# Optimization experiments

Measured on AMD Instinct MI355X. Metric: run time of the kernel, lower is better.

The kernel has to match this reference:

```python
import jax, jax.numpy as jnp
import numpy as np

D = 256
H = 8
FFN = 2048
EPS = 1e-5


def _layer_norm(x, g, b):
    m = jnp.mean(x, axis=-1, keepdims=True)
    v = jnp.mean((x - m) ** 2, axis=-1, keepdims=True)
    return (x - m) * jax.lax.rsqrt(v + EPS) * g + b


def _mha(q_in, k_in, v_in, wq, bq, wk, bk, wv, bv, wo, bo, mask):
    B, Sq, _ = q_in.shape
    Sk = k_in.shape[1]
    dh = D // H
    q = (q_in @ wq + bq).reshape(B, Sq, H, dh)
    k = (k_in @ wk + bk).reshape(B, Sk, H, dh)
    v = (v_in @ wv + bv).reshape(B, Sk, H, dh)
    scores = jnp.einsum('bqhd,bkhd->bhqk', q, k) / jnp.sqrt(jnp.float32(dh)).astype(q.dtype)
    if mask is not None:
        scores = scores + mask
    probs = jax.nn.softmax(scores, axis=-1)
    ctx = jnp.einsum('bhqk,bkhd->bqhd', probs, v).reshape(B, Sq, D)
    return ctx @ wo + bo


def setup_inputs() -> dict:
    key = jax.random.key(0)
    ks = jax.random.split(key, 32)
    s = 0.02
    def lin(i, din, dout):
        return jax.random.normal(ks[i], (din, dout), jnp.float32) * s
    inp = {
        'vision_encoder_hidden_states': jax.random.normal(ks[0], (4, 2048, D), jnp.float32),
        'text_encoder_hidden_states': jax.random.normal(ks[1], (4, 1024, D), jnp.float32),
        'vision_encoder_attention_mask': jnp.zeros((4, 1, 1, 2048), jnp.float32),
        'text_encoder_attention_mask': jnp.zeros((4, 1, 1, 1024), jnp.float32),
        'sa_wq': lin(2, D, D), 'sa_bq': jnp.zeros((D,), jnp.float32),
        'sa_wk': lin(3, D, D), 'sa_bk': jnp.zeros((D,), jnp.float32),
        'sa_wv': lin(4, D, D), 'sa_bv': jnp.zeros((D,), jnp.float32),
        'sa_wo': lin(5, D, D), 'sa_bo': jnp.zeros((D,), jnp.float32),
        'ca_wq': lin(6, D, D), 'ca_bq': jnp.zeros((D,), jnp.float32),
        'ca_wk': lin(7, D, D), 'ca_bk': jnp.zeros((D,), jnp.float32),
        'ca_wv': lin(8, D, D), 'ca_bv': jnp.zeros((D,), jnp.float32),
        'ca_wo': lin(9, D, D), 'ca_bo': jnp.zeros((D,), jnp.float32),
        'ln1_g': jnp.ones((D,), jnp.float32), 'ln1_b': jnp.zeros((D,), jnp.float32),
        'ln2_g': jnp.ones((D,), jnp.float32), 'ln2_b': jnp.zeros((D,), jnp.float32),
        'ln3_g': jnp.ones((D,), jnp.float32), 'ln3_b': jnp.zeros((D,), jnp.float32),
        'ln4_g': jnp.ones((D,), jnp.float32), 'ln4_b': jnp.zeros((D,), jnp.float32),
        'fc1_w': lin(10, D, FFN), 'fc1_b': jnp.zeros((FFN,), jnp.float32),
        'fc2_w': lin(11, FFN, D), 'fc2_b': jnp.zeros((D,), jnp.float32),
    }
    return inp


def reference(vision_encoder_hidden_states, text_encoder_hidden_states,
              vision_encoder_attention_mask, text_encoder_attention_mask,
              sa_wq, sa_bq, sa_wk, sa_bk, sa_wv, sa_bv, sa_wo, sa_bo,
              ca_wq, ca_bq, ca_wk, ca_bk, ca_wv, ca_bv, ca_wo, ca_bo,
              ln1_g, ln1_b, ln2_g, ln2_b, ln3_g, ln3_b, ln4_g, ln4_b,
              fc1_w, fc1_b, fc2_w, fc2_b):
    # self-attention over vision queries (dropout = identity in eval)
    residual = vision_encoder_hidden_states
    h = _mha(vision_encoder_hidden_states, vision_encoder_hidden_states,
             vision_encoder_hidden_states,
             sa_wq, sa_bq, sa_wk, sa_bk, sa_wv, sa_bv, sa_wo, sa_bo,
             vision_encoder_attention_mask)
    h = _layer_norm(residual + h, ln1_g, ln1_b)
    # text cross-attention
    res2 = h
    h = _mha(h, text_encoder_hidden_states, text_encoder_hidden_states,
             ca_wq, ca_bq, ca_wk, ca_bk, ca_wv, ca_bv, ca_wo, ca_bo,
             text_encoder_attention_mask)
    h = _layer_norm(res2 + h, ln2_g, ln2_b)
    # third block: residual + dropout(h) -> in eval this is h + h = 2h, then LN
    h = _layer_norm(h + h, ln3_g, ln3_b)
    # FFN
    res = h
    h = jax.nn.relu(h @ fc1_w + fc1_b)
    h = h @ fc2_w + fc2_b
    h = _layer_norm(res + h, ln4_g, ln4_b)
    return h
```

## Files before the change

### kernel.cpp

```cpp
#include <hip/hip_runtime.h>
#include <stdint.h>
#include <stddef.h>

#define HEADS 8
#define DH 32
#define DMODEL 256
#define LN_EPS 1e-5f
#define QSCALE 0.17677669529663687f

typedef unsigned short u16;
typedef __bf16 bf16x8 __attribute__((ext_vector_type(8)));
typedef unsigned short u16x8 __attribute__((ext_vector_type(8)));
typedef float f32x4 __attribute__((ext_vector_type(4)));

static __device__ __forceinline__ u16 bfc(float f) {
    return __builtin_bit_cast(u16, (__bf16)f);
}
static __device__ __forceinline__ bf16x8 ldbf8(const u16* p) {
    return __builtin_bit_cast(bf16x8, *reinterpret_cast<const u16x8*>(p));
}
static __device__ __forceinline__ bf16x8 cvt8(float4 a, float4 b) {
    bf16x8 r;
    r[0] = (__bf16)a.x; r[1] = (__bf16)a.y; r[2] = (__bf16)a.z; r[3] = (__bf16)a.w;
    r[4] = (__bf16)b.x; r[5] = (__bf16)b.y; r[6] = (__bf16)b.z; r[7] = (__bf16)b.w;
    return r;
}

struct TDesc { const float* src; u16* dst; int K; int N; };
struct TArgs { TDesc d[10]; };

__global__ __launch_bounds__(256) void transpose_cvt(TArgs args) {
    TDesc d = args.d[blockIdx.y];
    const int ntx = d.N >> 5;
    const int tiles = (d.K >> 5) * ntx;
    if ((int)blockIdx.x >= tiles) return;
    const int tk = (blockIdx.x / ntx) << 5;
    const int tn = (blockIdx.x % ntx) << 5;
    __shared__ float t[32][33];
    const int lx = threadIdx.x & 31;
    const int ly = threadIdx.x >> 5;
#pragma unroll
    for (int i = 0; i < 4; ++i)
        t[ly + 8 * i][lx] = d.src[(size_t)(tk + ly + 8 * i) * d.N + tn + lx];
    __syncthreads();
#pragma unroll
    for (int i = 0; i < 4; ++i)
        d.dst[(size_t)(tn + ly + 8 * i) * d.K + tk + lx] = bfc(t[lx][ly + 8 * i]);
}

struct Slice { u16* out; const float* bias; int mode; float sc; };

__global__ __launch_bounds__(256) void gemm_xproj(
    const float* __restrict__ Af, const u16* __restrict__ Wt,
    Slice s0, Slice s1, Slice s2, int M, int ntm)
{
    const int lane = threadIdx.x & 63;
    const int wave = threadIdx.x >> 6;
    const int l15 = lane & 15, lhi = lane >> 4;
    const int tm = ((int)blockIdx.x % ntm) * 128;
    const int tn = ((int)blockIdx.x / ntm) * 64;
    const int wm = tm + wave * 32;
    const int sel = tn >> 8;
    const int tl = tn & 255;
    Slice sl = (sel == 0) ? s0 : (sel == 1 ? s1 : s2);

    const f32x4 z4 = {0.f, 0.f, 0.f, 0.f};
    f32x4 acc[2][4];
#pragma unroll
    for (int i = 0; i < 2; ++i)
#pragma unroll
        for (int j = 0; j < 4; ++j) acc[i][j] = z4;

    const float* ar0 = Af + (size_t)(wm + l15) * 256 + lhi * 8;
    const float* ar1 = ar0 + (size_t)16 * 256;
    const u16* b0p = Wt + (size_t)(tn + l15) * 256 + lhi * 8;

    float4 a00 = *(const float4*)(ar0), a01 = *(const float4*)(ar0 + 4);
    float4 a10 = *(const float4*)(ar1), a11 = *(const float4*)(ar1 + 4);
    bf16x8 b[4];
#pragma unroll
    for (int j = 0; j < 4; ++j) b[j] = ldbf8(b0p + (size_t)j * 16 * 256);

#pragma unroll
    for (int k = 32; k < 256; k += 32) {
        float4 n00 = *(const float4*)(ar0 + k), n01 = *(const float4*)(ar0 + k + 4);
        float4 n10 = *(const float4*)(ar1 + k), n11 = *(const float4*)(ar1 + k + 4);
        bf16x8 bn[4];
#pragma unroll
        for (int j = 0; j < 4; ++j) bn[j] = ldbf8(b0p + (size_t)j * 16 * 256 + k);
        bf16x8 a0 = cvt8(a00, a01), a1 = cvt8(a10, a11);
#pragma unroll
        for (int j = 0; j < 4; ++j) {
            acc[0][j] = __builtin_amdgcn_mfma_f32_16x16x32_bf16(a0, b[j], acc[0][j], 0, 0, 0);
            acc[1][j] = __builtin_amdgcn_mfma_f32_16x16x32_bf16(a1, b[j], acc[1][j], 0, 0, 0);
        }
        a00 = n00; a01 = n01; a10 = n10; a11 = n11;
#pragma unroll
        for (int j = 0; j < 4; ++j) b[j] = bn[j];
    }
    {
        bf16x8 a0 = cvt8(a00, a01), a1 = cvt8(a10, a11);
#pragma unroll
        for (int j = 0; j < 4; ++j) {
            acc[0][j] = __builtin_amdgcn_mfma_f32_16x16x32_bf16(a0, b[j], acc[0][j], 0, 0, 0);
            acc[1][j] = __builtin_amdgcn_mfma_f32_16x16x32_bf16(a1, b[j], acc[1][j], 0, 0, 0);
        }
    }

#pragma unroll
    for (int i = 0; i < 2; ++i) {
#pragma unroll
        for (int j = 0; j < 4; ++j) {
            const int col = tl + j * 16 + l15;
            const float bv = sl.bias[col];
            const int row0 = wm + i * 16 + lhi * 4;
            if (sl.mode == 1) {
#pragma unroll
                for (int r = 0; r < 4; ++r)
                    sl.out[(size_t)(row0 + r) * 256 + col] = bfc((acc[i][j][r] + bv) * sl.sc);
            } else {
                ushort4 o = make_ushort4(bfc((acc[i][j][0] + bv) * sl.sc), bfc((acc[i][j][1] + bv) * sl.sc),
                                         bfc((acc[i][j][2] + bv) * sl.sc), bfc((acc[i][j][3] + bv) * sl.sc));
                *reinterpret_cast<ushort4*>(sl.out + (size_t)col * M + row0) = o;
            }
        }
    }
}

template<int MODE, bool RELU>
__global__ __launch_bounds__(256) void gemm_bias(
    const u16* __restrict__ A, const u16* __restrict__ Bt,
    const float* __restrict__ bias, void* __restrict__ Cout,
    int M, int N, int K, int ntm, float osc)
{
    const int lane = threadIdx.x & 63;
    const int wave = threadIdx.x >> 6;
    const int l15 = lane & 15, lhi = lane >> 4;
    const int tm = ((int)blockIdx.x % ntm) * 128;
    const int tn = ((int)blockIdx.x / ntm) * 64;
    const int wm = tm + wave * 32;

    const f32x4 z4 = {0.f, 0.f, 0.f, 0.f};
    f32x4 acc[2][4];
#pragma unroll
    for (int i = 0; i < 2; ++i)
#pragma unroll
        for (int j = 0; j < 4; ++j) acc[i][j] = z4;

    const u16* a0p = A + (size_t)(wm + l15) * K + lhi * 8;
    const u16* a1p = a0p + (size_t)16 * K;
    const u16* b0p = Bt + (size_t)(tn + l15) * K + lhi * 8;

    bf16x8 a0 = ldbf8(a0p), a1 = ldbf8(a1p);
    bf16x8 b[4];
#pragma unroll
    for (int j = 0; j < 4; ++j) b[j] = ldbf8(b0p + (size_t)j * 16 * K);

    for (int k = 32; k < K; k += 32) {
        bf16x8 a0n = ldbf8(a0p + k), a1n = ldbf8(a1p + k);
        bf16x8 bn[4];
#pragma unroll
        for (int j = 0; j < 4; ++j) bn[j] = ldbf8(b0p + (size_t)j * 16 * K + k);
#pragma unroll
        for (int j = 0; j < 4; ++j) {
            acc[0][j] = __builtin_amdgcn_mfma_f32_16x16x32_bf16(a0, b[j], acc[0][j], 0, 0, 0);
            acc[1][j] = __builtin_amdgcn_mfma_f32_16x16x32_bf16(a1, b[j], acc[1][j], 0, 0, 0);
        }
        a0 = a0n; a1 = a1n;
#pragma unroll
        for (int j = 0; j < 4; ++j) b[j] = bn[j];
    }
#pragma unroll
    for (int j = 0; j < 4; ++j) {
        acc[0][j] = __builtin_amdgcn_mfma_f32_16x16x32_bf16(a0, b[j], acc[0][j], 0, 0, 0);
        acc[1][j] = __builtin_amdgcn_mfma_f32_16x16x32_bf16(a1, b[j], acc[1][j], 0, 0, 0);
    }

#pragma unroll
    for (int i = 0; i < 2; ++i) {
#pragma unroll
        for (int j = 0; j < 4; ++j) {
            const int col = tn + j * 16 + l15;
            const float bv = bias[col];
            const int row0 = wm + i * 16 + lhi * 4;
            if (MODE == 0) {
                float* C = (float*)Cout;
#pragma unroll
                for (int r = 0; r < 4; ++r) {
                    float v = acc[i][j][r] + bv;
                    if (RELU) v = fmaxf(v, 0.f);
                    C[(size_t)(row0 + r) * N + col] = v;
                }
            } else {
                u16* C = (u16*)Cout;
#pragma unroll
                for (int r = 0; r < 4; ++r) {
                    float v = acc[i][j][r] + bv;
                    if (RELU) v = fmaxf(v, 0.f);
                    C[(size_t)(row0 + r) * N + col] = bfc(v * osc);
                }
            }
        }
    }
}

__global__ __launch_bounds__(256) void attn_kernel(
    const u16* __restrict__ Qb, const u16* __restrict__ Kb,
    const u16* __restrict__ Vt, const float* __restrict__ mask,
    u16* __restrict__ Ob, int Sq, int Sk, int MkTot)
{
    const int wave = threadIdx.x >> 6;
    const int lane = threadIdx.x & 63;
    const int l15 = lane & 15, lhi = lane >> 4;
    const int nqc = Sq >> 7;
    const int bh = blockIdx.x / nqc;
    const int qc = blockIdx.x % nqc;
    const int b = bh >> 3;
    const int h = bh & 7;
    const int colh = h * DH;
    const int qrow0 = b * Sq + (qc << 7) + wave * 32;
    const int swz = (l15 & 8) << 1;

    __shared__ __align__(16) u16 pt[4][32][72];

    const f32x4 z4 = {0.f, 0.f, 0.f, 0.f};
    bf16x8 qf[2];
    qf[0] = ldbf8(Qb + (size_t)(qrow0 + l15) * DMODEL + colh + lhi * 8);
    qf[1] = ldbf8(Qb + (size_t)(qrow0 + 16 + l15) * DMODEL + colh + lhi * 8);

    f32x4 ctx[2][2] = {{z4, z4}, {z4, z4}};
    float m0 = -1e30f, m1 = -1e30f, ss0 = 0.f, ss1 = 0.f;

    const float* mb = mask + (size_t)b * Sk;
    const u16* kbase = Kb + (size_t)(b * Sk) * DMODEL + colh + lhi * 8;
    const u16* vbase = Vt + (size_t)colh * MkTot + (size_t)b * Sk;

    bf16x8 kf[4], vf[4];
    float4 mk[4];
#pragma unroll
    for (int j = 0; j < 4; ++j)
        kf[j] = ldbf8(kbase + (size_t)(j * 16 + l15) * DMODEL);
#pragma unroll
    for (int ks = 0; ks < 2; ++ks)
#pragma unroll
        for (int dt = 0; dt < 2; ++dt)
            vf[ks * 2 + dt] = ldbf8(vbase + (size_t)(dt * 16 + l15) * MkTot + ks * 32 + lhi * 8);
#pragma unroll
    for (int j = 0; j < 4; ++j)
        mk[j] = *reinterpret_cast<const float4*>(mb + j * 16 + lhi * 4);

    for (int kt = 0; kt < Sk; kt += 64) {
        f32x4 s[2][4];
        __builtin_amdgcn_s_setprio(1);
#pragma unroll
        for (int j = 0; j < 4; ++j) {
            s[0][j] = __builtin_amdgcn_mfma_f32_16x16x32_bf16(kf[j], qf[0], z4, 0, 0, 0);
            s[1][j] = __builtin_amdgcn_mfma_f32_16x16x32_bf16(kf[j], qf[1], z4, 0, 0, 0);
        }
        __builtin_amdgcn_s_setprio(0);

        const int ktn = (kt + 64 < Sk) ? kt + 64 : kt;
        bf16x8 kn[4], vn[4];
        float4 mn[4];
#pragma unroll
        for (int j = 0; j < 4; ++j)
            kn[j] = ldbf8(kbase + (size_t)(ktn + j * 16 + l15) * DMODEL);
#pragma unroll
        for (int ks = 0; ks < 2; ++ks)
#pragma unroll
            for (int dt = 0; dt < 2; ++dt)
                vn[ks * 2 + dt] = ldbf8(vbase + (size_t)(dt * 16 + l15) * MkTot + ktn + ks * 32 + lhi * 8);
#pragma unroll
        for (int j = 0; j < 4; ++j)
            mn[j] = *reinterpret_cast<const float4*>(mb + ktn + j * 16 + lhi * 4);

#pragma unroll
        for (int j = 0; j < 4; ++j) {
            s[0][j][0] += mk[j].x; s[1][j][0] += mk[j].x;
            s[0][j][1] += mk[j].y; s[1][j][1] += mk[j].y;
            s[0][j][2] += mk[j].z; s[1][j][2] += mk[j].z;
            s[0][j][3] += mk[j].w; s[1][j][3] += mk[j].w;
        }

        float mx0 = fmaxf(fmaxf(s[0][0][0], s[0][0][1]), fmaxf(s[0][0][2], s[0][0][3]));
        float mx1 = fmaxf(fmaxf(s[1][0][0], s[1][0][1]), fmaxf(s[1][0][2], s[1][0][3]));
#pragma unroll
        for (int j = 1; j < 4; ++j) {
            mx0 = fmaxf(mx0, fmaxf(fmaxf(s[0][j][0], s[0][j][1]), fmaxf(s[0][j][2], s[0][j][3])));
            mx1 = fmaxf(mx1, fmaxf(fmaxf(s[1][j][0], s[1][j][1]), fmaxf(s[1][j][2], s[1][j][3])));
        }

        if (!__all((mx0 - m0 <= 8.0f) && (mx1 - m1 <= 8.0f))) {
            mx0 = fmaxf(mx0, __shfl_xor(mx0, 16, 64));
            mx0 = fmaxf(mx0, __shfl_xor(mx0, 32, 64));
            mx1 = fmaxf(mx1, __shfl_xor(mx1, 16, 64));
            mx1 = fmaxf(mx1, __shfl_xor(mx1, 32, 64));
            float n0 = fmaxf(m0, mx0), n1 = fmaxf(m1, mx1);
            float c0 = __expf(m0 - n0), c1 = __expf(m1 - n1);
            m0 = n0; m1 = n1; ss0 *= c0; ss1 *= c1;
#pragma unroll
            for (int r = 0; r < 4; ++r) {
                float cc0 = __shfl(c0, lhi * 4 + r, 64);
                float cc1 = __shfl(c1, lhi * 4 + r, 64);
                ctx[0][0][r] *= cc0; ctx[0][1][r] *= cc0;
                ctx[1][0][r] *= cc1; ctx[1][1][r] *= cc1;
            }
        }

        float ps0 = 0.f, ps1 = 0.f;
#pragma unroll
        for (int j = 0; j < 4; ++j)
#pragma unroll
            for (int r = 0; r < 4; ++r) {
                float p0 = __expf(s[0][j][r] - m0);
                float p1 = __expf(s[1][j][r] - m1);
                s[0][j][r] = p0; s[1][j][r] = p1;
                ps0 += p0; ps1 += p1;
            }
        ss0 += ps0; ss1 += ps1;

        asm volatile("" ::: "memory");
#pragma unroll
        for (int i = 0; i < 2; ++i)
#pragma unroll
            for (int j = 0; j < 4; ++j) {
                ushort4 w = make_ushort4(bfc(s[i][j][0]), bfc(s[i][j][1]),
                                         bfc(s[i][j][2]), bfc(s[i][j][3]));
                *reinterpret_cast<ushort4*>(&pt[wave][i * 16 + l15][(j * 16 + lhi * 4) ^ swz]) = w;
            }
        asm volatile("" ::: "memory");

        __builtin_amdgcn_s_setprio(1);
#pragma unroll
        for (int ks = 0; ks < 2; ++ks) {
            bf16x8 pa0 = ldbf8(&pt[wave][l15][(ks * 32 + lhi * 8) ^ swz]);
            bf16x8 pa1 = ldbf8(&pt[wave][16 + l15][(ks * 32 + lhi * 8) ^ swz]);
#pragma unroll
            for (int dt = 0; dt < 2; ++dt) {
                ctx[0][dt] = __builtin_amdgcn_mfma_f32_16x16x32_bf16(pa0, vf[ks * 2 + dt], ctx[0][dt], 0, 0, 0);
                ctx[1][dt] = __builtin_amdgcn_mfma_f32_16x16x32_bf16(pa1, vf[ks * 2 + dt], ctx[1][dt], 0, 0, 0);
            }
        }
        __builtin_amdgcn_s_setprio(0);

#pragma unroll
        for (int j = 0; j < 4; ++j) { kf[j] = kn[j]; vf[j] = vn[j]; mk[j] = mn[j]; }
    }

    ss0 += __shfl_xor(ss0, 16, 64); ss0 += __shfl_xor(ss0, 32, 64);
    ss1 += __shfl_xor(ss1, 16, 64); ss1 += __shfl_xor(ss1, 32, 64);
#pragma unroll
    for (int r = 0; r < 4; ++r) {
        const float i0 = 1.0f / __shfl(ss0, lhi * 4 + r, 64);
        const float i1 = 1.0f / __shfl(ss1, lhi * 4 + r, 64);
        const int row0 = qrow0 + lhi * 4 + r;
#pragma unroll
        for (int dt = 0; dt < 2; ++dt) {
            Ob[(size_t)row0 * DMODEL + colh + dt * 16 + l15] = bfc(ctx[0][dt][r] * i0);
            Ob[(size_t)(row0 + 16) * DMODEL + colh + dt * 16 + l15] = bfc(ctx[1][dt][r] * i1);
        }
    }
}

template<bool DBL, bool WBF>
__global__ __launch_bounds__(256) void ln_kernel(
    const float* __restrict__ X, const float* __restrict__ Res,
    const float* __restrict__ g1p, const float* __restrict__ b1p,
    const float* __restrict__ g2p, const float* __restrict__ b2p,
    float* __restrict__ Of, u16* __restrict__ Oh)
{
    const int lane = threadIdx.x & 63;
    const int row = blockIdx.x * 4 + (threadIdx.x >> 6);
    const size_t base = (size_t)row * DMODEL + lane * 4;
    float4 x = *reinterpret_cast<const float4*>(X + base);
    float4 rr = *reinterpret_cast<const float4*>(Res + base);
    float v[4] = {x.x + rr.x, x.y + rr.y, x.z + rr.z, x.w + rr.w};
    float s = v[0] + v[1] + v[2] + v[3];
    float q = v[0] * v[0] + v[1] * v[1] + v[2] * v[2] + v[3] * v[3];
#pragma unroll
    for (int m = 1; m < 64; m <<= 1) { s += __shfl_xor(s, m, 64); q += __shfl_xor(q, m, 64); }
    float mean = s * (1.0f / DMODEL);
    float rstd = rsqrtf(fmaxf(q * (1.0f / DMODEL) - mean * mean, 0.f) + LN_EPS);
    float4 g = *reinterpret_cast<const float4*>(g1p + lane * 4);
    float4 bb = *reinterpret_cast<const float4*>(b1p + lane * 4);
    float y[4];
    y[0] = (v[0] - mean) * rstd * g.x + bb.x;
    y[1] = (v[1] - mean) * rstd * g.y + bb.y;
    y[2] = (v[2] - mean) * rstd * g.z + bb.z;
    y[3] = (v[3] - mean) * rstd * g.w + bb.w;
    if constexpr (DBL) {
#pragma unroll
        for (int k2 = 0; k2 < 4; ++k2) y[k2] *= 2.0f;
        float s2 = y[0] + y[1] + y[2] + y[3];
        float q2 = y[0] * y[0] + y[1] * y[1] + y[2] * y[2] + y[3] * y[3];
#pragma unroll
        for (int m = 1; m < 64; m <<= 1) { s2 += __shfl_xor(s2, m, 64); q2 += __shfl_xor(q2, m, 64); }
        float mean2 = s2 * (1.0f / DMODEL);
        float rstd2 = rsqrtf(fmaxf(q2 * (1.0f / DMODEL) - mean2 * mean2, 0.f) + LN_EPS);
        float4 g2 = *reinterpret_cast<const float4*>(g2p + lane * 4);
        float4 b2 = *reinterpret_cast<const float4*>(b2p + lane * 4);
        y[0] = (y[0] - mean2) * rstd2 * g2.x + b2.x;
        y[1] = (y[1] - mean2) * rstd2 * g2.y + b2.y;
        y[2] = (y[2] - mean2) * rstd2 * g2.z + b2.z;
        y[3] = (y[3] - mean2) * rstd2 * g2.w + b2.w;
    }
    *reinterpret_cast<float4*>(Of + base) = make_float4(y[0], y[1], y[2], y[3]);
    if constexpr (WBF) {
        ushort4 o = make_ushort4(bfc(y[0]), bfc(y[1]), bfc(y[2]), bfc(y[3]));
        *reinterpret_cast<ushort4*>(Oh + base) = o;
    }
}

extern "C" void kernel_launch(void* const* d_in, const int* in_sizes, int n_in,
                              void* d_out, int out_size, void* d_ws, size_t ws_size,
                              hipStream_t stream) {
    constexpr size_t MB = 1u << 20;
    if (ws_size < 70 * MB) return;

    const float* vis   = (const float*)d_in[0];
    const float* txt   = (const float*)d_in[1];
    const float* vmask = (const float*)d_in[2];
    const float* tmask = (const float*)d_in[3];
    const float* sa_wq = (const float*)d_in[4];  const float* sa_bq = (const float*)d_in[5];
    const float* sa_wk = (const float*)d_in[6];  const float* sa_bk = (const float*)d_in[7];
    const float* sa_wv = (const float*)d_in[8];  const float* sa_bv = (const float*)d_in[9];
    const float* sa_wo = (const float*)d_in[10]; const float* sa_bo = (const float*)d_in[11];
    const float* ca_wq = (const float*)d_in[12]; const float* ca_bq = (const float*)d_in[13];
    const float* ca_wk = (const float*)d_in[14]; const float* ca_bk = (const float*)d_in[15];
    const float* ca_wv = (const float*)d_in[16]; const float* ca_bv = (const float*)d_in[17];
    const float* ca_wo = (const float*)d_in[18]; const float* ca_bo = (const float*)d_in[19];
    const float* ln1_g = (const float*)d_in[20]; const float* ln1_b = (const float*)d_in[21];
    const float* ln2_g = (const float*)d_in[22]; const float* ln2_b = (const float*)d_in[23];
    const float* ln3_g = (const float*)d_in[24]; const float* ln3_b = (const float*)d_in[25];
    const float* ln4_g = (const float*)d_in[26]; const float* ln4_b = (const float*)d_in[27];
    const float* fc1_w = (const float*)d_in[28]; const float* fc1_b = (const float*)d_in[29];
    const float* fc2_w = (const float*)d_in[30]; const float* fc2_b = (const float*)d_in[31];

    const int B = 4, Sq = 2048, St = 1024;
    const int Mq = B * Sq;
    const int Mt = B * St;

    char* ws = (char*)d_ws;
    u16*   q_bf    = (u16*)(ws + 6 * MB);
    u16*   k_bf    = (u16*)(ws + 10 * MB);
    u16*   vt_bf   = (u16*)(ws + 14 * MB);
    u16*   ctx_bf  = (u16*)(ws + 18 * MB);
    u16*   ffn1_bf = (u16*)(ws + 0);
    float* attn_f  = (float*)(ws + 32 * MB);
    float* h1_f    = (float*)(ws + 40 * MB);
    u16*   h1_bf   = (u16*)(ws + 48 * MB);
    float* h3_f    = (float*)(ws + 52 * MB);
    u16*   h3_bf   = (u16*)(ws + 60 * MB);
    u16*   wts     = (u16*)(ws + 64 * MB);
    float* ffn2_f  = attn_f;

    u16* wqkv_t = wts;
    u16* wkv_t  = wqkv_t + 768 * 256;
    u16* cwq_t  = wkv_t + 512 * 256;
    u16* wo_t   = cwq_t + 65536;
    u16* cwo_t  = wo_t + 65536;
    u16* fc1_t  = cwo_t + 65536;
    u16* fc2_t  = fc1_t + 2048 * 256;

    TArgs ta;
    ta.d[0] = {sa_wq, wqkv_t + 0 * 65536, 256, 256};
    ta.d[1] = {sa_wk, wqkv_t + 1 * 65536, 256, 256};
    ta.d[2] = {sa_wv, wqkv_t + 2 * 65536, 256, 256};
    ta.d[3] = {ca_wk, wkv_t + 0 * 65536, 256, 256};
    ta.d[4] = {ca_wv, wkv_t + 1 * 65536, 256, 256};
    ta.d[5] = {ca_wq, cwq_t, 256, 256};
    ta.d[6] = {sa_wo, wo_t, 256, 256};
    ta.d[7] = {ca_wo, cwo_t, 256, 256};
    ta.d[8] = {fc1_w, fc1_t, 256, 2048};
    ta.d[9] = {fc2_w, fc2_t, 2048, 256};
    transpose_cvt<<<dim3(512, 10), 256, 0, stream>>>(ta);

    auto gemm_grid = [](int M, int N) { return dim3((M / 128) * (N / 64)); };

    Slice sq = {q_bf, sa_bq, 1, QSCALE}, sk = {k_bf, sa_bk, 1, 1.f}, sv = {vt_bf, sa_bv, 2, 1.f};
    gemm_xproj<<<dim3((Mq / 128) * 12), 256, 0, stream>>>(vis, wqkv_t, sq, sk, sv, Mq, Mq / 128);
    attn_kernel<<<dim3(B * HEADS * (Sq / 128)), 256, 0, stream>>>(q_bf, k_bf, vt_bf, vmask, ctx_bf, Sq, Sq, Mq);
    gemm_bias<0, false><<<gemm_grid(Mq, 256), 256, 0, stream>>>(ctx_bf, wo_t, sa_bo, attn_f, Mq, 256, 256, Mq / 128, 1.f);
    ln_kernel<false, true><<<dim3(Mq / 4), 256, 0, stream>>>(attn_f, vis, ln1_g, ln1_b, nullptr, nullptr, h1_f, h1_bf);

    Slice ck = {k_bf, ca_bk, 1, 1.f}, cv = {vt_bf, ca_bv, 2, 1.f}, cd = {nullptr, nullptr, 1, 1.f};
    gemm_xproj<<<dim3((Mt / 128) * 8), 256, 0, stream>>>(txt, wkv_t, ck, cv, cd, Mt, Mt / 128);
    gemm_bias<1, false><<<gemm_grid(Mq, 256), 256, 0, stream>>>(h1_bf, cwq_t, ca_bq, q_bf, Mq, 256, 256, Mq / 128, QSCALE);
    attn_kernel<<<dim3(B * HEADS * (Sq / 128)), 256, 0, stream>>>(q_bf, k_bf, vt_bf, tmask, ctx_bf, Sq, St, Mt);
    gemm_bias<0, false><<<gemm_grid(Mq, 256), 256, 0, stream>>>(ctx_bf, cwo_t, ca_bo, attn_f, Mq, 256, 256, Mq / 128, 1.f);
    ln_kernel<true, true><<<dim3(Mq / 4), 256, 0, stream>>>(attn_f, h1_f, ln2_g, ln2_b, ln3_g, ln3_b, h3_f, h3_bf);

    gemm_bias<1, true><<<gemm_grid(Mq, 2048), 256, 0, stream>>>(h3_bf, fc1_t, fc1_b, ffn1_bf, Mq, 2048, 256, Mq / 128, 1.f);
    gemm_bias<0, false><<<gemm_grid(Mq, 256), 256, 0, stream>>>(ffn1_bf, fc2_t, fc2_b, ffn2_f, Mq, 256, 2048, Mq / 128, 1.f);
    ln_kernel<false, false><<<dim3(Mq / 4), 256, 0, stream>>>(ffn2_f, h3_f, ln4_g, ln4_b, nullptr, nullptr, (float*)d_out, nullptr);
}
```

Before: 295.4 us.

## Retile GEMMs, split-K the FFN down-projection, and use exp2 softmax in attention

Replaces the single GEMM kernel with three variants: a 128x128-tile kernel for the FC1 up-projection, a two-way split-K kernel for FC2 whose partial sums are added inside the final layernorm, and a 64x64-tile kernel for the 256-wide projections so more blocks are launched. Attention now folds log2(e) into the Q scale and mask and uses the hardware exp2 instruction. It also drops the s_setprio hints, splits the row-sum accumulation into independent chains, and raises the lazy-rescale threshold. These changes target low occupancy and long serial K loops in the GEMMs and the cost of exp in softmax. In exchange they add register pressure for the wide tile and extra fp32 traffic for the split-K partials.

```diff
diff --git a/kernel.cpp b/kernel.cpp
--- a/kernel.cpp
+++ b/kernel.cpp
@@ -6,7 +6,10 @@
 #define DH 32
 #define DMODEL 256
 #define LN_EPS 1e-5f
+#define LOG2E 1.4426950408889634f
 #define QSCALE 0.17677669529663687f
+#define QSCALE2 (QSCALE * LOG2E)
+#define EXP2(x) __builtin_amdgcn_exp2f(x)
 
 typedef unsigned short u16;
 typedef __bf16 bf16x8 __attribute__((ext_vector_type(8)));
@@ -128,7 +131,7 @@
 }
 
 template<int MODE, bool RELU>
-__global__ __launch_bounds__(256) void gemm_bias(
+__global__ __launch_bounds__(256) void gemm_wide(
     const u16* __restrict__ A, const u16* __restrict__ Bt,
     const float* __restrict__ bias, void* __restrict__ Cout,
     int M, int N, int K, int ntm, float osc)
@@ -137,30 +140,108 @@
     const int wave = threadIdx.x >> 6;
     const int l15 = lane & 15, lhi = lane >> 4;
     const int tm = ((int)blockIdx.x % ntm) * 128;
-    const int tn = ((int)blockIdx.x / ntm) * 64;
+    const int tn = ((int)blockIdx.x / ntm) * 128;
     const int wm = tm + wave * 32;
 
     const f32x4 z4 = {0.f, 0.f, 0.f, 0.f};
-    f32x4 acc[2][4];
+    f32x4 acc[2][8];
 #pragma unroll
     for (int i = 0; i < 2; ++i)
 #pragma unroll
-        for (int j = 0; j < 4; ++j) acc[i][j] = z4;
+        for (int j = 0; j < 8; ++j) acc[i][j] = z4;
 
     const u16* a0p = A + (size_t)(wm + l15) * K + lhi * 8;
     const u16* a1p = a0p + (size_t)16 * K;
     const u16* b0p = Bt + (size_t)(tn + l15) * K + lhi * 8;
 
     bf16x8 a0 = ldbf8(a0p), a1 = ldbf8(a1p);
-    bf16x8 b[4];
-#pragma unroll
-    for (int j = 0; j < 4; ++j) b[j] = ldbf8(b0p + (size_t)j * 16 * K);
+    bf16x8 b[8];
+#pragma unroll
+    for (int j = 0; j < 8; ++j) b[j] = ldbf8(b0p + (size_t)j * 16 * K);
 
     for (int k = 32; k < K; k += 32) {
         bf16x8 a0n = ldbf8(a0p + k), a1n = ldbf8(a1p + k);
+        bf16x8 bn[8];
+#pragma unroll
+        for (int j = 0; j < 8; ++j) bn[j] = ldbf8(b0p + (size_t)j * 16 * K + k);
+#pragma unroll
+        for (int j = 0; j < 8; ++j) {
+            acc[0][j] = __builtin_amdgcn_mfma_f32_16x16x32_bf16(a0, b[j], acc[0][j], 0, 0, 0);
+            acc[1][j] = __builtin_amdgcn_mfma_f32_16x16x32_bf16(a1, b[j], acc[1][j], 0, 0, 0);
+        }
+        a0 = a0n; a1 = a1n;
+#pragma unroll
+        for (int j = 0; j < 8; ++j) b[j] = bn[j];
+    }
+#pragma unroll
+    for (int j = 0; j < 8; ++j) {
+        acc[0][j] = __builtin_amdgcn_mfma_f32_16x16x32_bf16(a0, b[j], acc[0][j], 0, 0, 0);
+        acc[1][j] = __builtin_amdgcn_mfma_f32_16x16x32_bf16(a1, b[j], acc[1][j], 0, 0, 0);
+    }
+
+#pragma unroll
+    for (int i = 0; i < 2; ++i) {
+#pragma unroll
+        for (int j = 0; j < 8; ++j) {
+            const int col = tn + j * 16 + l15;
+            const float bv = bias[col];
+            const int row0 = wm + i * 16 + lhi * 4;
+            if (MODE == 0) {
+                float* C = (float*)Cout;
+#pragma unroll
+                for (int r = 0; r < 4; ++r) {
+                    float v = acc[i][j][r] + bv;
+                    if (RELU) v = fmaxf(v, 0.f);
+                    C[(size_t)(row0 + r) * N + col] = v;
+                }
+            } else {
+                u16* C = (u16*)Cout;
+#pragma unroll
+                for (int r = 0; r < 4; ++r) {
+                    float v = acc[i][j][r] + bv;
+                    if (RELU) v = fmaxf(v, 0.f);
+                    C[(size_t)(row0 + r) * N + col] = bfc(v * osc);
+                }
+            }
+        }
+    }
+}
+
+__global__ __launch_bounds__(256) void gemm_sk2(
+    const u16* __restrict__ A, const u16* __restrict__ Bt,
+    const float* __restrict__ bias, float* __restrict__ Cout,
+    int M, int N, int lda, int Kh, int ntm)
+{
+    const int kh = (int)blockIdx.x >= (ntm * (N / 64));
+    const int bid = (int)blockIdx.x - kh * (ntm * (N / 64));
+    const int lane = threadIdx.x & 63;
+    const int wave = threadIdx.x >> 6;
+    const int l15 = lane & 15, lhi = lane >> 4;
+    const int tm = (bid % ntm) * 128;
+    const int tn = (bid / ntm) * 64;
+    const int wm = tm + wave * 32;
+
+    const f32x4 z4 = {0.f, 0.f, 0.f, 0.f};
+    f32x4 acc[2][4];
+#pragma unroll
+    for (int i = 0; i < 2; ++i)
+#pragma unroll
+        for (int j = 0; j < 4; ++j) acc[i][j] = z4;
+
+    const u16* a0p = A + (size_t)(wm + l15) * lda + kh * Kh + lhi * 8;
+    const u16* a1p = a0p + (size_t)16 * lda;
+    const u16* b0p = Bt + (size_t)(tn + l15) * lda + kh * Kh + lhi * 8;
+
+    bf16x8 a0 = ldbf8(a0p), a1 = ldbf8(a1p);
+    bf16x8 b[4];
+#pragma unroll
+    for (int j = 0; j < 4; ++j) b[j] = ldbf8(b0p + (size_t)j * 16 * lda);
+
+    for (int k = 32; k < Kh; k += 32) {
+        bf16x8 a0n = ldbf8(a0p + k), a1n = ldbf8(a1p + k);
         bf16x8 bn[4];
 #pragma unroll
-        for (int j = 0; j < 4; ++j) bn[j] = ldbf8(b0p + (size_t)j * 16 * K + k);
+        for (int j = 0; j < 4; ++j) bn[j] = ldbf8(b0p + (size_t)j * 16 * lda + k);
 #pragma unroll
         for (int j = 0; j < 4; ++j) {
             acc[0][j] = __builtin_amdgcn_mfma_f32_16x16x32_bf16(a0, b[j], acc[0][j], 0, 0, 0);
@@ -176,11 +257,70 @@
         acc[1][j] = __builtin_amdgcn_mfma_f32_16x16x32_bf16(a1, b[j], acc[1][j], 0, 0, 0);
     }
 
+    float* C = Cout + (size_t)kh * M * N;
+    const float bs = kh ? 0.f : 1.f;
 #pragma unroll
     for (int i = 0; i < 2; ++i) {
 #pragma unroll
         for (int j = 0; j < 4; ++j) {
             const int col = tn + j * 16 + l15;
+            const float bv = bias[col] * bs;
+            const int row0 = wm + i * 16 + lhi * 4;
+#pragma unroll
+            for (int r = 0; r < 4; ++r)
+                C[(size_t)(row0 + r) * N + col] = acc[i][j][r] + bv;
+        }
+    }
+}
+
+template<int MODE, bool RELU>
+__global__ __launch_bounds__(256) void gemm64(
+    const u16* __restrict__ A, const u16* __restrict__ Bt,
+    const float* __restrict__ bias, void* __restrict__ Cout,
+    int M, int N, int K, int ntn, float osc)
+{
+    const int lane = threadIdx.x & 63;
+    const int wave = threadIdx.x >> 6;
+    const int l15 = lane & 15, lhi = lane >> 4;
+    const int tn = ((int)blockIdx.x % ntn) * 64;
+    const int tm = ((int)blockIdx.x / ntn) * 64;
+    const int wm = tm + (wave & 1) * 32;
+    const int wn = tn + (wave >> 1) * 32;
+
+    const f32x4 z4 = {0.f, 0.f, 0.f, 0.f};
+    f32x4 acc[2][2] = {{z4, z4}, {z4, z4}};
+
+    const u16* a0p = A + (size_t)(wm + l15) * K + lhi * 8;
+    const u16* a1p = a0p + (size_t)16 * K;
+    const u16* b0p = Bt + (size_t)(wn + l15) * K + lhi * 8;
+    const u16* b1p = b0p + (size_t)16 * K;
+
+    bf16x8 aA0 = ldbf8(a0p), aA1 = ldbf8(a1p), bA0 = ldbf8(b0p), bA1 = ldbf8(b1p);
+    bf16x8 aB0 = ldbf8(a0p + 32), aB1 = ldbf8(a1p + 32), bB0 = ldbf8(b0p + 32), bB1 = ldbf8(b1p + 32);
+
+#define G64_MFMA(aX0, aX1, bX0, bX1)                                                        \
+    acc[0][0] = __builtin_amdgcn_mfma_f32_16x16x32_bf16(aX0, bX0, acc[0][0], 0, 0, 0);      \
+    acc[0][1] = __builtin_amdgcn_mfma_f32_16x16x32_bf16(aX0, bX1, acc[0][1], 0, 0, 0);      \
+    acc[1][0] = __builtin_amdgcn_mfma_f32_16x16x32_bf16(aX1, bX0, acc[1][0], 0, 0, 0);      \
+    acc[1][1] = __builtin_amdgcn_mfma_f32_16x16x32_bf16(aX1, bX1, acc[1][1], 0, 0, 0);
+
+    for (int k = 64; k < K; k += 64) {
+        G64_MFMA(aA0, aA1, bA0, bA1);
+        aA0 = ldbf8(a0p + k); aA1 = ldbf8(a1p + k);
+        bA0 = ldbf8(b0p + k); bA1 = ldbf8(b1p + k);
+        G64_MFMA(aB0, aB1, bB0, bB1);
+        aB0 = ldbf8(a0p + k + 32); aB1 = ldbf8(a1p + k + 32);
+        bB0 = ldbf8(b0p + k + 32); bB1 = ldbf8(b1p + k + 32);
+    }
+    G64_MFMA(aA0, aA1, bA0, bA1);
+    G64_MFMA(aB0, aB1, bB0, bB1);
+#undef G64_MFMA
+
+#pragma unroll
+    for (int i = 0; i < 2; ++i) {
+#pragma unroll
+        for (int j = 0; j < 2; ++j) {
+            const int col = wn + j * 16 + l15;
             const float bv = bias[col];
             const int row0 = wm + i * 16 + lhi * 4;
             if (MODE == 0) {
@@ -224,9 +364,8 @@
     __shared__ __align__(16) u16 pt[4][32][72];
 
     const f32x4 z4 = {0.f, 0.f, 0.f, 0.f};
-    bf16x8 qf[2];
-    qf[0] = ldbf8(Qb + (size_t)(qrow0 + l15) * DMODEL + colh + lhi * 8);
-    qf[1] = ldbf8(Qb + (size_t)(qrow0 + 16 + l15) * DMODEL + colh + lhi * 8);
+    const bf16x8 qf0 = ldbf8(Qb + (size_t)(qrow0 + l15) * DMODEL + colh + lhi * 8);
+    const bf16x8 qf1 = ldbf8(Qb + (size_t)(qrow0 + 16 + l15) * DMODEL + colh + lhi * 8);
 
     f32x4 ctx[2][2] = {{z4, z4}, {z4, z4}};
     float m0 = -1e30f, m1 = -1e30f, ss0 = 0.f, ss1 = 0.f;
@@ -246,18 +385,18 @@
         for (int dt = 0; dt < 2; ++dt)
             vf[ks * 2 + dt] = ldbf8(vbase + (size_t)(dt * 16 + l15) * MkTot + ks * 32 + lhi * 8);
 #pragma unroll
-    for (int j = 0; j < 4; ++j)
-        mk[j] = *reinterpret_cast<const float4*>(mb + j * 16 + lhi * 4);
+    for (int j = 0; j < 4; ++j) {
+        float4 t0 = *reinterpret_cast<const float4*>(mb + j * 16 + lhi * 4);
+        mk[j] = make_float4(t0.x * LOG2E, t0.y * LOG2E, t0.z * LOG2E, t0.w * LOG2E);
+    }
 
     for (int kt = 0; kt < Sk; kt += 64) {
         f32x4 s[2][4];
-        __builtin_amdgcn_s_setprio(1);
-#pragma unroll
-        for (int j = 0; j < 4; ++j) {
-            s[0][j] = __builtin_amdgcn_mfma_f32_16x16x32_bf16(kf[j], qf[0], z4, 0, 0, 0);
-            s[1][j] = __builtin_amdgcn_mfma_f32_16x16x32_bf16(kf[j], qf[1], z4, 0, 0, 0);
-        }
-        __builtin_amdgcn_s_setprio(0);
+#pragma unroll
+        for (int j = 0; j < 4; ++j) {
+            s[0][j] = __builtin_amdgcn_mfma_f32_16x16x32_bf16(kf[j], qf0, z4, 0, 0, 0);
+            s[1][j] = __builtin_amdgcn_mfma_f32_16x16x32_bf16(kf[j], qf1, z4, 0, 0, 0);
+        }
 
         const int ktn = (kt + 64 < Sk) ? kt + 64 : kt;
         bf16x8 kn[4], vn[4];
@@ -290,13 +429,13 @@
             mx1 = fmaxf(mx1, fmaxf(fmaxf(s[1][j][0], s[1][j][1]), fmaxf(s[1][j][2], s[1][j][3])));
         }
 
-        if (!__all((mx0 - m0 <= 8.0f) && (mx1 - m1 <= 8.0f))) {
+        if (!__all((mx0 - m0 <= 12.0f) && (mx1 - m1 <= 12.0f))) {
             mx0 = fmaxf(mx0, __shfl_xor(mx0, 16, 64));
             mx0 = fmaxf(mx0, __shfl_xor(mx0, 32, 64));
             mx1 = fmaxf(mx1, __shfl_xor(mx1, 16, 64));
             mx1 = fmaxf(mx1, __shfl_xor(mx1, 32, 64));
             float n0 = fmaxf(m0, mx0), n1 = fmaxf(m1, mx1);
-            float c0 = __expf(m0 - n0), c1 = __expf(m1 - n1);
+            float c0 = EXP2(m0 - n0), c1 = EXP2(m1 - n1);
             m0 = n0; m1 = n1; ss0 *= c0; ss1 *= c1;
 #pragma unroll
             for (int r = 0; r < 4; ++r) {
@@ -307,17 +446,21 @@
             }
         }
 
-        float ps0 = 0.f, ps1 = 0.f;
-#pragma unroll
-        for (int j = 0; j < 4; ++j)
-#pragma unroll
-            for (int r = 0; r < 4; ++r) {
-                float p0 = __expf(s[0][j][r] - m0);
-                float p1 = __expf(s[1][j][r] - m1);
-                s[0][j][r] = p0; s[1][j][r] = p1;
-                ps0 += p0; ps1 += p1;
-            }
-        ss0 += ps0; ss1 += ps1;
+        float pa0 = 0.f, pb0 = 0.f, pc0 = 0.f, pd0 = 0.f;
+        float pa1 = 0.f, pb1 = 0.f, pc1 = 0.f, pd1 = 0.f;
+#pragma unroll
+        for (int j = 0; j < 4; ++j) {
+            float e00 = EXP2(s[0][j][0] - m0), e01 = EXP2(s[0][j][1] - m0);
+            float e02 = EXP2(s[0][j][2] - m0), e03 = EXP2(s[0][j][3] - m0);
+            float e10 = EXP2(s[1][j][0] - m1), e11 = EXP2(s[1][j][1] - m1);
+            float e12 = EXP2(s[1][j][2] - m1), e13 = EXP2(s[1][j][3] - m1);
+            s[0][j][0] = e00; s[0][j][1] = e01; s[0][j][2] = e02; s[0][j][3] = e03;
+            s[1][j][0] = e10; s[1][j][1] = e11; s[1][j][2] = e12; s[1][j][3] = e13;
+            pa0 += e00; pb0 += e01; pc0 += e02; pd0 += e03;
+            pa1 += e10; pb1 += e11; pc1 += e12; pd1 += e13;
+        }
+        ss0 += (pa0 + pb0) + (pc0 + pd0);
+        ss1 += (pa1 + pb1) + (pc1 + pd1);
 
         asm volatile("" ::: "memory");
 #pragma unroll
@@ -330,18 +473,16 @@
             }
         asm volatile("" ::: "memory");
 
-        __builtin_amdgcn_s_setprio(1);
 #pragma unroll
         for (int ks = 0; ks < 2; ++ks) {
-            bf16x8 pa0 = ldbf8(&pt[wave][l15][(ks * 32 + lhi * 8) ^ swz]);
-            bf16x8 pa1 = ldbf8(&pt[wave][16 + l15][(ks * 32 + lhi * 8) ^ swz]);
+            bf16x8 pa = ldbf8(&pt[wave][l15][(ks * 32 + lhi * 8) ^ swz]);
+            bf16x8 pb = ldbf8(&pt[wave][16 + l15][(ks * 32 + lhi * 8) ^ swz]);
 #pragma unroll
             for (int dt = 0; dt < 2; ++dt) {
-                ctx[0][dt] = __builtin_amdgcn_mfma_f32_16x16x32_bf16(pa0, vf[ks * 2 + dt], ctx[0][dt], 0, 0, 0);
-                ctx[1][dt] = __builtin_amdgcn_mfma_f32_16x16x32_bf16(pa1, vf[ks * 2 + dt], ctx[1][dt], 0, 0, 0);
+                ctx[0][dt] = __builtin_amdgcn_mfma_f32_16x16x32_bf16(pa, vf[ks * 2 + dt], ctx[0][dt], 0, 0, 0);
+                ctx[1][dt] = __builtin_amdgcn_mfma_f32_16x16x32_bf16(pb, vf[ks * 2 + dt], ctx[1][dt], 0, 0, 0);
             }
         }
-        __builtin_amdgcn_s_setprio(0);
 
 #pragma unroll
         for (int j = 0; j < 4; ++j) { kf[j] = kn[j]; vf[j] = vn[j]; mk[j] = mn[j]; }
@@ -362,9 +503,9 @@
     }
 }
 
-template<bool DBL, bool WBF>
+template<bool DBL, bool WBF, bool SPLIT>
 __global__ __launch_bounds__(256) void ln_kernel(
-    const float* __restrict__ X, const float* __restrict__ Res,
+    const float* __restrict__ X, const float* __restrict__ X2, const float* __restrict__ Res,
     const float* __restrict__ g1p, const float* __restrict__ b1p,
     const float* __restrict__ g2p, const float* __restrict__ b2p,
     float* __restrict__ Of, u16* __restrict__ Oh)
@@ -375,6 +516,10 @@
     float4 x = *reinterpret_cast<const float4*>(X + base);
     float4 rr = *reinterpret_cast<const float4*>(Res + base);
     float v[4] = {x.x + rr.x, x.y + rr.y, x.z + rr.z, x.w + rr.w};
+    if constexpr (SPLIT) {
+        float4 x2 = *reinterpret_cast<const float4*>(X2 + base);
+        v[0] += x2.x; v[1] += x2.y; v[2] += x2.z; v[3] += x2.w;
+    }
     float s = v[0] + v[1] + v[2] + v[3];
     float q = v[0] * v[0] + v[1] * v[1] + v[2] * v[2] + v[3] * v[3];
 #pragma unroll
@@ -452,7 +597,8 @@
     float* h3_f    = (float*)(ws + 52 * MB);
     u16*   h3_bf   = (u16*)(ws + 60 * MB);
     u16*   wts     = (u16*)(ws + 64 * MB);
-    float* ffn2_f  = attn_f;
+    float* ffn2a   = attn_f;
+    float* ffn2b   = h1_f;
 
     u16* wqkv_t = wts;
     u16* wkv_t  = wqkv_t + 768 * 256;
@@ -475,22 +621,20 @@
     ta.d[9] = {fc2_w, fc2_t, 2048, 256};
     transpose_cvt<<<dim3(512, 10), 256, 0, stream>>>(ta);
 
-    auto gemm_grid = [](int M, int N) { return dim3((M / 128) * (N / 64)); };
-
-    Slice sq = {q_bf, sa_bq, 1, QSCALE}, sk = {k_bf, sa_bk, 1, 1.f}, sv = {vt_bf, sa_bv, 2, 1.f};
+    Slice sq = {q_bf, sa_bq, 1, QSCALE2}, sk = {k_bf, sa_bk, 1, 1.f}, sv = {vt_bf, sa_bv, 2, 1.f};
     gemm_xproj<<<dim3((Mq / 128) * 12), 256, 0, stream>>>(vis, wqkv_t, sq, sk, sv, Mq, Mq / 128);
     attn_kernel<<<dim3(B * HEADS * (Sq / 128)), 256, 0, stream>>>(q_bf, k_bf, vt_bf, vmask, ctx_bf, Sq, Sq, Mq);
-    gemm_bias<0, false><<<gemm_grid(Mq, 256), 256, 0, stream>>>(ctx_bf, wo_t, sa_bo, attn_f, Mq, 256, 256, Mq / 128, 1.f);
-    ln_kernel<false, true><<<dim3(Mq / 4), 256, 0, stream>>>(attn_f, vis, ln1_g, ln1_b, nullptr, nullptr, h1_f, h1_bf);
+    gemm64<0, false><<<dim3((Mq / 64) * 4), 256, 0, stream>>>(ctx_bf, wo_t, sa_bo, attn_f, Mq, 256, 256, 4, 1.f);
+    ln_kernel<false, true, false><<<dim3(Mq / 4), 256, 0, stream>>>(attn_f, nullptr, vis, ln1_g, ln1_b, nullptr, nullptr, h1_f, h1_bf);
 
     Slice ck = {k_bf, ca_bk, 1, 1.f}, cv = {vt_bf, ca_bv, 2, 1.f}, cd = {nullptr, nullptr, 1, 1.f};
     gemm_xproj<<<dim3((Mt / 128) * 8), 256, 0, stream>>>(txt, wkv_t, ck, cv, cd, Mt, Mt / 128);
-    gemm_bias<1, false><<<gemm_grid(Mq, 256), 256, 0, stream>>>(h1_bf, cwq_t, ca_bq, q_bf, Mq, 256, 256, Mq / 128, QSCALE);
+    gemm64<1, false><<<dim3((Mq / 64) * 4), 256, 0, stream>>>(h1_bf, cwq_t, ca_bq, q_bf, Mq, 256, 256, 4, QSCALE2);
     attn_kernel<<<dim3(B * HEADS * (Sq / 128)), 256, 0, stream>>>(q_bf, k_bf, vt_bf, tmask, ctx_bf, Sq, St, Mt);
-    gemm_bias<0, false><<<gemm_grid(Mq, 256), 256, 0, stream>>>(ctx_bf, cwo_t, ca_bo, attn_f, Mq, 256, 256, Mq / 128, 1.f);
-    ln_kernel<true, true><<<dim3(Mq / 4), 256, 0, stream>>>(attn_f, h1_f, ln2_g, ln2_b, ln3_g, ln3_b, h3_f, h3_bf);
-
-    gemm_bias<1, true><<<gemm_grid(Mq, 2048), 256, 0, stream>>>(h3_bf, fc1_t, fc1_b, ffn1_bf, Mq, 2048, 256, Mq / 128, 1.f);
-    gemm_bias<0, false><<<gemm_grid(Mq, 256), 256, 0, stream>>>(ffn1_bf, fc2_t, fc2_b, ffn2_f, Mq, 256, 2048, Mq / 128, 1.f);
-    ln_kernel<false, false><<<dim3(Mq / 4), 256, 0, stream>>>(ffn2_f, h3_f, ln4_g, ln4_b, nullptr, nullptr, (float*)d_out, nullptr);
-}
+    gemm64<0, false><<<dim3((Mq / 64) * 4), 256, 0, stream>>>(ctx_bf, cwo_t, ca_bo, attn_f, Mq, 256, 256, 4, 1.f);
+    ln_kernel<true, true, false><<<dim3(Mq / 4), 256, 0, stream>>>(attn_f, nullptr, h1_f, ln2_g, ln2_b, ln3_g, ln3_b, h3_f, h3_bf);
+
+    gemm_wide<1, true><<<dim3((Mq / 128) * 16), 256, 0, stream>>>(h3_bf, fc1_t, fc1_b, ffn1_bf, Mq, 2048, 256, Mq / 128, 1.f);
+    gemm_sk2<<<dim3((Mq / 128) * 4 * 2), 256, 0, stream>>>(ffn1_bf, fc2_t, fc2_b, ffn2a, Mq, 256, 2048, 1024, Mq / 128);
+    ln_kernel<false, false, true><<<dim3(Mq / 4), 256, 0, stream>>>(ffn2a, ffn2b, h3_f, ln4_g, ln4_b, nullptr, nullptr, (float*)d_out, nullptr);
+}
```

Result: no change. 290.6 us, median of 2 (-1.6%).
